# Kernel optimization log

Hardware: AMD Instinct MI355X
Metric: run time of the kernel (lower is better)

The kernel has to match this reference:

```python
import jax, jax.numpy as jnp
import numpy as np

TOP_K = 2
EPS = 1e-9


def setup_inputs() -> dict:
    key = jax.random.key(0)
    k1, k2, k3, k4 = jax.random.split(key, 4)
    B, T, D, H, E = 4, 2048, 1024, 4096, 8
    x = jax.random.normal(k1, (B, T, D), dtype=jnp.float32)
    Wr = jax.random.normal(k2, (D, E), dtype=jnp.float32) * 0.02
    W1 = jax.random.normal(k3, (E, D, H), dtype=jnp.float32) * 0.02
    W2 = jax.random.normal(k4, (E, H, D), dtype=jnp.float32) * 0.02
    return {"x": x, "Wr": Wr, "W1": W1, "W2": W2}


def reference(x, Wr, W1, W2):
    # x: (B,T,D); Wr: (D,E); W1: (E,D,H); W2: (E,H,D)
    E = Wr.shape[1]
    logits = jnp.einsum('btd,de->bte', x, Wr)          # (B,T,E)
    probs = jax.nn.softmax(logits, axis=-1)
    top_p, top_i = jax.lax.top_k(probs, TOP_K)         # (B,T,K)
    gates = top_p / (jnp.sum(top_p, axis=-1, keepdims=True) + EPS)
    # combine weights per expert: (B,T,E), zero where expert not selected
    oh = jax.nn.one_hot(top_i, E, dtype=x.dtype)       # (B,T,K,E)
    comb = jnp.sum(oh * gates[..., None], axis=2)      # (B,T,E)
    out = jnp.zeros_like(x)
    for e in range(E):  # fixed small expert loop
        h = jax.nn.gelu(jnp.einsum('btd,dh->bth', x, W1[e]), approximate=False)
        y = jnp.einsum('bth,hd->btd', h, W2[e])
        out = out + comb[..., e:e + 1] * y
    # load-balancing loss (on detached stats, matching torch .detach())
    mask = (jnp.sum(oh, axis=2) > 0).astype(jnp.float32)  # (B,T,E)
    imp = jnp.sum(jax.lax.stop_gradient(probs), axis=(0, 1))
    load = jnp.sum(jax.lax.stop_gradient(mask), axis=(0, 1))
    imp = imp / (jnp.sum(imp) + EPS)
    load = load / (jnp.sum(load) + EPS)
    lb = jnp.sum(imp * load) * E
    return out, lb
```

## Files before the change

kernel.cpp:

```cpp
#include <hip/hip_runtime.h>
#include <hip/hip_bf16.h>
#include <math.h>

#define NTOK 8192
#define DDIM 1024
#define HDIM 4096
#define NEXP 8
#define HROWS (NTOK*2 + 256)
#define RBLK 512

typedef unsigned int u32;
typedef unsigned short u16;
typedef __bf16 bf16x8 __attribute__((ext_vector_type(8)));
typedef float f32x4 __attribute__((ext_vector_type(4)));
typedef u16 u16x8 __attribute__((ext_vector_type(8)));
typedef u16 u16x4 __attribute__((ext_vector_type(4)));

__device__ __forceinline__ u16 f2bf(float f){
  u32 u = __builtin_bit_cast(u32, f);
  u32 r = (u + 0x7FFFu + ((u >> 16) & 1u)) >> 16;
  return (u16)r;
}
__device__ __forceinline__ float bf2f(u16 b){
  u32 u = ((u32)b) << 16;
  return __builtin_bit_cast(float, u);
}
__device__ __forceinline__ void gl_lds16(const void* g, void* l){
  __builtin_amdgcn_global_load_lds(
      (const __attribute__((address_space(1))) u32*)g,
      (__attribute__((address_space(3))) u32*)l, 16, 0, 0);
}
__device__ __forceinline__ float gelu_t(float v){
  float u = v * (0.7978845608f + 0.0356774081f * v * v);
  float e = __expf(2.0f * u);
  float t = 1.0f - 2.0f / (e + 1.0f);
  return 0.5f * v * (1.0f + t);
}

__global__ __launch_bounds__(256) void cvtx_kernel(const float* __restrict__ x,
                                                   u16* __restrict__ xb){
  long i = (long)(blockIdx.x * 256 + threadIdx.x) * 8;
  float4 a = *(const float4*)(x + i);
  float4 b = *(const float4*)(x + i + 4);
  u16x8 o;
  o[0]=f2bf(a.x); o[1]=f2bf(a.y); o[2]=f2bf(a.z); o[3]=f2bf(a.w);
  o[4]=f2bf(b.x); o[5]=f2bf(b.y); o[6]=f2bf(b.z); o[7]=f2bf(b.w);
  *(u16x8*)(xb + i) = o;
}

__global__ __launch_bounds__(256) void transpose_cvt(const float* __restrict__ in,
                                                     u16* __restrict__ out,
                                                     int R, int C){
  int e = blockIdx.z;
  const float* pin = in + (long)e * R * C;
  u16* pout = out + (long)e * R * C;
  __shared__ u16 tile[64][65];
  int c0 = blockIdx.x * 64, r0 = blockIdx.y * 64;
  int tid = threadIdx.x;
#pragma unroll
  for (int j = 0; j < 16; j++){
    int idx = tid + 256 * j;
    int r = idx >> 6, c = idx & 63;
    tile[r][c] = f2bf(pin[(long)(r0 + r) * C + c0 + c]);
  }
  __syncthreads();
#pragma unroll
  for (int j = 0; j < 16; j++){
    int idx = tid + 256 * j;
    int r = idx >> 6, c = idx & 63;
    pout[(long)(c0 + r) * R + r0 + c] = tile[c][r];
  }
}

__global__ __launch_bounds__(1024) void route_kernel(const float* __restrict__ x,
                                                     const float* __restrict__ Wr,
                                                     int4* __restrict__ meta,
                                                     float2* __restrict__ gates,
                                                     int* __restrict__ selrk,
                                                     int* __restrict__ blockhist,
                                                     float* __restrict__ impPart){
  const int wid = threadIdx.x >> 6;
  const int lane = threadIdx.x & 63;
  const int t = blockIdx.x * 16 + wid;
  const float* xr = x + (long)t * DDIM;
  float acc[NEXP] = {};
  for (int d0 = lane * 4; d0 < DDIM; d0 += 256){
    float4 xv = *(const float4*)(xr + d0);
    const float* w = Wr + d0 * NEXP;
#pragma unroll
    for (int q = 0; q < 4; q++){
      float xq = ((const float*)&xv)[q];
      float4 w0 = *(const float4*)(w + q * NEXP);
      float4 w1 = *(const float4*)(w + q * NEXP + 4);
      acc[0] += xq * w0.x; acc[1] += xq * w0.y; acc[2] += xq * w0.z; acc[3] += xq * w0.w;
      acc[4] += xq * w1.x; acc[5] += xq * w1.y; acc[6] += xq * w1.z; acc[7] += xq * w1.w;
    }
  }
#pragma unroll
  for (int e = 0; e < NEXP; e++){
#pragma unroll
    for (int off = 32; off; off >>= 1) acc[e] += __shfl_xor(acc[e], off, 64);
  }
  __shared__ int sel_s[32];
  __shared__ float p_s[16][NEXP];
  if (lane == 0){
    float mx = acc[0];
#pragma unroll
    for (int e = 1; e < NEXP; e++) mx = fmaxf(mx, acc[e]);
    float p[NEXP]; float s = 0.f;
#pragma unroll
    for (int e = 0; e < NEXP; e++){ p[e] = expf(acc[e] - mx); s += p[e]; }
    float inv = 1.f / s;
#pragma unroll
    for (int e = 0; e < NEXP; e++){ p[e] *= inv; p_s[wid][e] = p[e]; }
    int i0 = 0; float v0 = p[0];
#pragma unroll
    for (int e = 1; e < NEXP; e++) if (p[e] > v0){ v0 = p[e]; i0 = e; }
    int i1 = -1; float v1 = -1.f;
#pragma unroll
    for (int e = 0; e < NEXP; e++) if (e != i0 && p[e] > v1){ v1 = p[e]; i1 = e; }
    float gs = v0 + v1 + 1e-9f;
    meta[t] = make_int4(i0, i1, 0, 0);
    gates[t] = make_float2(v0 / gs, v1 / gs);
    sel_s[wid * 2] = i0;
    sel_s[wid * 2 + 1] = i1;
  }
  __syncthreads();
  const int tid = threadIdx.x;
  if (tid < 32){
    int e = sel_s[tid];
    int r = 0;
    for (int m = 0; m < tid; m++) r += (sel_s[m] == e) ? 1 : 0;
    selrk[blockIdx.x * 32 + tid] = (r << 3) | e;
  }
  if (tid < NEXP){
    int hcount = 0;
#pragma unroll
    for (int m = 0; m < 32; m++) hcount += (sel_s[m] == tid) ? 1 : 0;
    blockhist[blockIdx.x * NEXP + tid] = hcount;
    float s = 0.f;
#pragma unroll
    for (int w = 0; w < 16; w++) s += p_s[w][tid];
    impPart[blockIdx.x * NEXP + tid] = s;
  }
}

__global__ __launch_bounds__(512) void scan_kernel(int* __restrict__ blockhist,
                                                   const float* __restrict__ impPart,
                                                   int* __restrict__ cnt,
                                                   int* __restrict__ offs,
                                                   float* __restrict__ imp){
  const int e = threadIdx.x >> 6;
  const int lane = threadIdx.x & 63;
  const int base = lane * 8;
  int v[8]; int s = 0;
#pragma unroll
  for (int i = 0; i < 8; i++){
    int tmp = blockhist[(base + i) * NEXP + e];
    v[i] = s; s += tmp;
  }
  int inc = s;
#pragma unroll
  for (int off = 1; off < 64; off <<= 1){
    int o = __shfl_up(inc, off, 64);
    if (lane >= off) inc += o;
  }
  int excl = inc - s;
#pragma unroll
  for (int i = 0; i < 8; i++) blockhist[(base + i) * NEXP + e] = v[i] + excl;
  int tot = __shfl(inc, 63, 64);
  float fs = 0.f;
#pragma unroll
  for (int i = 0; i < 8; i++) fs += impPart[(base + i) * NEXP + e];
#pragma unroll
  for (int off = 32; off; off >>= 1) fs += __shfl_xor(fs, off, 64);
  __shared__ int cnt_s[NEXP];
  if (lane == 0){ cnt_s[e] = tot; cnt[e] = tot; imp[e] = fs; }
  __syncthreads();
  if (threadIdx.x == 0){
    int o = 0;
    for (int q = 0; q < NEXP; q++){ offs[q] = o; o += cnt_s[q]; }
  }
}

__global__ __launch_bounds__(256) void fill_kernel(const int* __restrict__ selrk,
                                                   const int* __restrict__ blockhist,
                                                   int* __restrict__ elist,
                                                   int4* __restrict__ meta){
  int m = blockIdx.x * 256 + threadIdx.x;
  int t = m >> 1, c = m & 1, b = m >> 5;
  int pk = selrk[m];
  int e = pk & 7, r = pk >> 3;
  int gslot = blockhist[b * NEXP + e] + r;
  elist[e * NTOK + gslot] = t;
  ((int*)meta)[t * 4 + 2 + c] = gslot;
}

template<int KD, int ND, bool GATHER, bool GELU>
__global__ __launch_bounds__(256) void gemm128_kernel(const u16* __restrict__ Ag,
                                                      const u16* __restrict__ Bg,
                                                      u16* __restrict__ Cg,
                                                      const int* __restrict__ elist,
                                                      const int* __restrict__ cnt,
                                                      const int* __restrict__ offs){
  const int e = blockIdx.z;
  const int n_e = cnt[e];
  const int tt = blockIdx.y;
  if (tt * 128 >= n_e) return;
  const int cb = blockIdx.x * 128;
  __shared__ __align__(16) u16 As[128 * 64];
  __shared__ __align__(16) u16 Bs[128 * 64];
  const int tid = threadIdx.x;
  const int csrc = (((tid & 7) ^ ((tid >> 3) & 7)) << 3);
  const int clin = (tid & 7) << 3;
  const int row0 = offs[e] + tt * 128;
  const long bbase = ((long)e * ND + cb) * KD;
  long agb[4], bgb[4]; int lrow[4];
#pragma unroll
  for (int q = 0; q < 4; q++){
    int row = q * 32 + (tid >> 3);
    int arow;
    if (GATHER){
      int slot = tt * 128 + row;
      if (slot >= n_e) slot = n_e - 1;
      arow = elist[e * NTOK + slot];
    } else {
      arow = row0 + row;
    }
    lrow[q] = row;
    agb[q] = (long)arow * KD + csrc;
    bgb[q] = bbase + (long)row * KD + csrc;
  }
  const int wid = tid >> 6, lane = tid & 63;
  const int wr = (wid >> 1) * 64, wc = (wid & 1) * 64;
  const int fr = lane & 15, fq = lane >> 4;
  const int sw0 = (fq ^ (fr & 7)) << 3;
  const int sw1 = ((4 + fq) ^ (fr & 7)) << 3;
  const u16* aP0 = &As[(wr + fr) * 64 + sw0];
  const u16* aP1 = &As[(wr + fr) * 64 + sw1];
  const u16* bP0 = &Bs[(wc + fr) * 64 + sw0];
  const u16* bP1 = &Bs[(wc + fr) * 64 + sw1];
  f32x4 acc[4][4] = {};
  for (int kb = 0; kb < KD; kb += 64){
    __syncthreads();
#pragma unroll
    for (int q = 0; q < 4; q++){
      gl_lds16(Ag + agb[q] + kb, &As[lrow[q] * 64 + clin]);
      gl_lds16(Bg + bgb[q] + kb, &Bs[lrow[q] * 64 + clin]);
    }
    __syncthreads();
    {
      bf16x8 af[4], bfr[4];
#pragma unroll
      for (int m = 0; m < 4; m++) af[m] = *(const bf16x8*)(aP0 + m * 1024);
#pragma unroll
      for (int n = 0; n < 4; n++) bfr[n] = *(const bf16x8*)(bP0 + n * 1024);
#pragma unroll
      for (int m = 0; m < 4; m++)
#pragma unroll
        for (int n = 0; n < 4; n++)
          acc[m][n] = __builtin_amdgcn_mfma_f32_16x16x32_bf16(af[m], bfr[n], acc[m][n], 0, 0, 0);
    }
    {
      bf16x8 af[4], bfr[4];
#pragma unroll
      for (int m = 0; m < 4; m++) af[m] = *(const bf16x8*)(aP1 + m * 1024);
#pragma unroll
      for (int n = 0; n < 4; n++) bfr[n] = *(const bf16x8*)(bP1 + n * 1024);
#pragma unroll
      for (int m = 0; m < 4; m++)
#pragma unroll
        for (int n = 0; n < 4; n++)
          acc[m][n] = __builtin_amdgcn_mfma_f32_16x16x32_bf16(af[m], bfr[n], acc[m][n], 0, 0, 0);
    }
  }
#pragma unroll
  for (int m = 0; m < 4; m++){
#pragma unroll
    for (int j = 0; j < 4; j++){
      int row = wr + m * 16 + fq * 4 + j;
      int slot = tt * 128 + row;
      if (slot >= n_e) continue;
      long base = (long)(row0 + row) * ND + cb + wc;
#pragma unroll
      for (int n = 0; n < 4; n++){
        float v = acc[m][n][j];
        if (GELU) v = gelu_t(v);
        Cg[base + n * 16 + fr] = f2bf(v);
      }
    }
  }
}

__global__ __launch_bounds__(256) void combine_kernel(const u16* __restrict__ ypair,
                                                      const int4* __restrict__ meta,
                                                      const float2* __restrict__ gates,
                                                      const int* __restrict__ offs,
                                                      float* __restrict__ out){
  int t = blockIdx.x;
  int c = threadIdx.x;
  int4 m = meta[t];
  float2 g = gates[t];
  long p0 = (long)(offs[m.x] + m.z) * DDIM + c * 4;
  long p1 = (long)(offs[m.y] + m.w) * DDIM + c * 4;
  u16x4 y0 = *(const u16x4*)&ypair[p0];
  u16x4 y1 = *(const u16x4*)&ypair[p1];
  float4 o;
  o.x = g.x * bf2f(y0[0]) + g.y * bf2f(y1[0]);
  o.y = g.x * bf2f(y0[1]) + g.y * bf2f(y1[1]);
  o.z = g.x * bf2f(y0[2]) + g.y * bf2f(y1[2]);
  o.w = g.x * bf2f(y0[3]) + g.y * bf2f(y1[3]);
  *(float4*)&out[(long)t * DDIM + c * 4] = o;
}

__global__ void lb_kernel(const float* __restrict__ imp, const int* __restrict__ cnt,
                          float* __restrict__ outp){
  if (threadIdx.x == 0 && blockIdx.x == 0){
    float si = 0.f, sl = 0.f;
    for (int e = 0; e < NEXP; e++){ si += imp[e]; sl += (float)cnt[e]; }
    float lb = 0.f;
    for (int e = 0; e < NEXP; e++)
      lb += (imp[e] / (si + 1e-9f)) * ((float)cnt[e] / (sl + 1e-9f));
    outp[0] = lb * (float)NEXP;
  }
}

extern "C" void kernel_launch(void* const* d_in, const int* in_sizes, int n_in,
                              void* d_out, int out_size, void* d_ws, size_t ws_size,
                              hipStream_t stream){
  const float* x  = (const float*)d_in[0];
  const float* Wr = (const float*)d_in[1];
  const float* W1 = (const float*)d_in[2];
  const float* W2 = (const float*)d_in[3];
  float* out = (float*)d_out;
  char* ws = (char*)d_ws;
  size_t off = 0;
  u16* xb = (u16*)(ws + off);   off += (size_t)NTOK * DDIM * 2;
  u16* wt = (u16*)(ws + off);   off += (size_t)NEXP * DDIM * HDIM * 2;
  u16* h  = (u16*)(ws + off);   off += (size_t)HROWS * HDIM * 2;
  u16* yp = (u16*)(ws + off);   off += (size_t)NTOK * 2 * DDIM * 2;
  int* elist    = (int*)(ws + off);    off += (size_t)NEXP * NTOK * 4;
  int4* meta    = (int4*)(ws + off);   off += (size_t)NTOK * 16;
  float2* gts   = (float2*)(ws + off); off += (size_t)NTOK * 8;
  int* selrk    = (int*)(ws + off);    off += (size_t)NTOK * 2 * 4;
  int* bhist    = (int*)(ws + off);    off += (size_t)RBLK * NEXP * 4;
  float* impP   = (float*)(ws + off);  off += (size_t)RBLK * NEXP * 4;
  int* cnt      = (int*)(ws + off);    off += 32;
  float* imp    = (float*)(ws + off);  off += 32;
  int* offs     = (int*)(ws + off);    off += 32;
  if (ws_size < off) return;

  cvtx_kernel<<<4096, 256, 0, stream>>>(x, xb);
  route_kernel<<<RBLK, 1024, 0, stream>>>(x, Wr, meta, gts, selrk, bhist, impP);
  scan_kernel<<<1, 512, 0, stream>>>(bhist, impP, cnt, offs, imp);
  fill_kernel<<<NTOK * 2 / 256, 256, 0, stream>>>(selrk, bhist, elist, meta);
  transpose_cvt<<<dim3(HDIM / 64, DDIM / 64, NEXP), 256, 0, stream>>>(W1, wt, DDIM, HDIM);
  gemm128_kernel<DDIM, HDIM, true, true><<<dim3(HDIM / 128, NTOK / 128, NEXP), 256, 0, stream>>>(
      xb, wt, h, elist, cnt, offs);
  transpose_cvt<<<dim3(DDIM / 64, HDIM / 64, NEXP), 256, 0, stream>>>(W2, wt, HDIM, DDIM);
  gemm128_kernel<HDIM, DDIM, false, false><<<dim3(DDIM / 128, NTOK / 128, NEXP), 256, 0, stream>>>(
      h, wt, yp, elist, cnt, offs);
  combine_kernel<<<NTOK, 256, 0, stream>>>(yp, meta, gts, offs, out);
  lb_kernel<<<1, 64, 0, stream>>>(imp, cnt, out + (size_t)NTOK * DDIM);
}
```

Measured before the change: 542.2 us.

## Fuse x bf16 conversion into router, vectorize weight transpose, interleave expert GEMM blocks

```diff
diff --git a/kernel.cpp b/kernel.cpp
--- a/kernel.cpp
+++ b/kernel.cpp
@@ -35,17 +35,6 @@
   float e = __expf(2.0f * u);
   float t = 1.0f - 2.0f / (e + 1.0f);
   return 0.5f * v * (1.0f + t);
-}
-
-__global__ __launch_bounds__(256) void cvtx_kernel(const float* __restrict__ x,
-                                                   u16* __restrict__ xb){
-  long i = (long)(blockIdx.x * 256 + threadIdx.x) * 8;
-  float4 a = *(const float4*)(x + i);
-  float4 b = *(const float4*)(x + i + 4);
-  u16x8 o;
-  o[0]=f2bf(a.x); o[1]=f2bf(a.y); o[2]=f2bf(a.z); o[3]=f2bf(a.w);
-  o[4]=f2bf(b.x); o[5]=f2bf(b.y); o[6]=f2bf(b.z); o[7]=f2bf(b.w);
-  *(u16x8*)(xb + i) = o;
 }
 
 __global__ __launch_bounds__(256) void transpose_cvt(const float* __restrict__ in,
@@ -58,22 +47,30 @@
   int c0 = blockIdx.x * 64, r0 = blockIdx.y * 64;
   int tid = threadIdx.x;
 #pragma unroll
-  for (int j = 0; j < 16; j++){
+  for (int j = 0; j < 4; j++){
     int idx = tid + 256 * j;
-    int r = idx >> 6, c = idx & 63;
-    tile[r][c] = f2bf(pin[(long)(r0 + r) * C + c0 + c]);
+    int r = idx >> 4, c4 = (idx & 15) << 2;
+    float4 v = *(const float4*)(pin + (long)(r0 + r) * C + c0 + c4);
+    tile[r][c4]     = f2bf(v.x);
+    tile[r][c4 + 1] = f2bf(v.y);
+    tile[r][c4 + 2] = f2bf(v.z);
+    tile[r][c4 + 3] = f2bf(v.w);
   }
   __syncthreads();
 #pragma unroll
-  for (int j = 0; j < 16; j++){
+  for (int j = 0; j < 4; j++){
     int idx = tid + 256 * j;
-    int r = idx >> 6, c = idx & 63;
-    pout[(long)(c0 + r) * R + r0 + c] = tile[c][r];
+    int orow = idx >> 4, c4 = (idx & 15) << 2;
+    u16x4 o;
+    o[0] = tile[c4][orow];     o[1] = tile[c4 + 1][orow];
+    o[2] = tile[c4 + 2][orow]; o[3] = tile[c4 + 3][orow];
+    *(u16x4*)(pout + (long)(c0 + orow) * R + r0 + c4) = o;
   }
 }
 
 __global__ __launch_bounds__(1024) void route_kernel(const float* __restrict__ x,
                                                      const float* __restrict__ Wr,
+                                                     u16* __restrict__ xb,
                                                      int4* __restrict__ meta,
                                                      float2* __restrict__ gates,
                                                      int* __restrict__ selrk,
@@ -83,9 +80,13 @@
   const int lane = threadIdx.x & 63;
   const int t = blockIdx.x * 16 + wid;
   const float* xr = x + (long)t * DDIM;
+  u16* xbr = xb + (long)t * DDIM;
   float acc[NEXP] = {};
   for (int d0 = lane * 4; d0 < DDIM; d0 += 256){
     float4 xv = *(const float4*)(xr + d0);
+    u16x4 xo;
+    xo[0] = f2bf(xv.x); xo[1] = f2bf(xv.y); xo[2] = f2bf(xv.z); xo[3] = f2bf(xv.w);
+    *(u16x4*)(xbr + d0) = xo;
     const float* w = Wr + d0 * NEXP;
 #pragma unroll
     for (int q = 0; q < 4; q++){
@@ -203,11 +204,15 @@
                                                       const int* __restrict__ elist,
                                                       const int* __restrict__ cnt,
                                                       const int* __restrict__ offs){
-  const int e = blockIdx.z;
+  const int NDB = ND / 128;
+  const int bid = blockIdx.x;
+  const int e  = bid & 7;
+  const int le = bid >> 3;
+  const int db = le % NDB;
+  const int tt = le / NDB;
   const int n_e = cnt[e];
-  const int tt = blockIdx.y;
   if (tt * 128 >= n_e) return;
-  const int cb = blockIdx.x * 128;
+  const int cb = db * 128;
   __shared__ __align__(16) u16 As[128 * 64];
   __shared__ __align__(16) u16 Bs[128 * 64];
   const int tid = threadIdx.x;
@@ -350,15 +355,14 @@
   int* offs     = (int*)(ws + off);    off += 32;
   if (ws_size < off) return;
 
-  cvtx_kernel<<<4096, 256, 0, stream>>>(x, xb);
-  route_kernel<<<RBLK, 1024, 0, stream>>>(x, Wr, meta, gts, selrk, bhist, impP);
+  route_kernel<<<RBLK, 1024, 0, stream>>>(x, Wr, xb, meta, gts, selrk, bhist, impP);
   scan_kernel<<<1, 512, 0, stream>>>(bhist, impP, cnt, offs, imp);
   fill_kernel<<<NTOK * 2 / 256, 256, 0, stream>>>(selrk, bhist, elist, meta);
   transpose_cvt<<<dim3(HDIM / 64, DDIM / 64, NEXP), 256, 0, stream>>>(W1, wt, DDIM, HDIM);
-  gemm128_kernel<DDIM, HDIM, true, true><<<dim3(HDIM / 128, NTOK / 128, NEXP), 256, 0, stream>>>(
+  gemm128_kernel<DDIM, HDIM, true, true><<<NEXP * (NTOK / 128) * (HDIM / 128), 256, 0, stream>>>(
       xb, wt, h, elist, cnt, offs);
   transpose_cvt<<<dim3(DDIM / 64, HDIM / 64, NEXP), 256, 0, stream>>>(W2, wt, HDIM, DDIM);
-  gemm128_kernel<HDIM, DDIM, false, false><<<dim3(DDIM / 128, NTOK / 128, NEXP), 256, 0, stream>>>(
+  gemm128_kernel<HDIM, DDIM, false, false><<<NEXP * (NTOK / 128) * (DDIM / 128), 256, 0, stream>>>(
       h, wt, yp, elist, cnt, offs);
   combine_kernel<<<NTOK, 256, 0, stream>>>(yp, meta, gts, offs, out);
   lb_kernel<<<1, 64, 0, stream>>>(imp, cnt, out + (size_t)NTOK * DDIM);
```

Result: no change. 531.6 us (-2.0%).
